# Kernel tuning notes

Measured on AMD Instinct MI355X. Metric: run time of the kernel, lower is better.

## Reference

```python
import jax, jax.numpy as jnp
from jax import lax
import numpy as np

H = 20  # hidden_size


def _lstm_layer(x, Wih, Whh, bih, bhh):
    # x: [B, T, D_in]; Wih: [4H, D_in]; Whh: [4H, H]
    B = x.shape[0]
    b = bih + bhh  # [4H]

    def step(carry, xt):
        h, c = carry
        gates = xt @ Wih.T + h @ Whh.T + b  # [B, 4H]
        i, f, g, o = jnp.split(gates, 4, axis=-1)  # torch gate order: i,f,g,o
        i = jax.nn.sigmoid(i)
        f = jax.nn.sigmoid(f)
        g = jnp.tanh(g)
        o = jax.nn.sigmoid(o)
        c = f * c + i * g
        h = o * jnp.tanh(c)
        return (h, c), h

    h0 = jnp.zeros((B, H), x.dtype)
    c0 = jnp.zeros((B, H), x.dtype)
    (_, _), hs = lax.scan(step, (h0, c0), jnp.swapaxes(x, 0, 1))  # hs: [T, B, H]
    return jnp.swapaxes(hs, 0, 1)  # [B, T, H]


def setup_inputs() -> dict:
    key = jax.random.key(0)
    ks = jax.random.split(key, 11)
    B, T, D = 4096, 512, 1
    s = 1.0 / np.sqrt(H)  # torch LSTM init scale
    u = lambda k, shp: jax.random.uniform(k, shp, jnp.float32, -s, s)
    return {
        "x": jax.random.normal(ks[0], (B, T, D), jnp.float32),
        "Wih0": u(ks[1], (4 * H, D)),
        "Whh0": u(ks[2], (4 * H, H)),
        "bih0": u(ks[3], (4 * H,)),
        "bhh0": u(ks[4], (4 * H,)),
        "Wih1": u(ks[5], (4 * H, H)),
        "Whh1": u(ks[6], (4 * H, H)),
        "bih1": u(ks[7], (4 * H,)),
        "bhh1": u(ks[8], (4 * H,)),
        "fcW": u(ks[9], (1, H)),
        "fcb": u(ks[10], (1,)),
    }


def reference(x, Wih0, Whh0, bih0, bhh0, Wih1, Whh1, bih1, bhh1, fcW, fcb):
    h1 = _lstm_layer(x, Wih0, Whh0, bih0, bhh0)   # [B, T, H]
    h2 = _lstm_layer(h1, Wih1, Whh1, bih1, bhh1)  # [B, T, H]
    # self.drop is defined but never applied in the original forward
    return h2[:, -1, :] @ fcW.T + fcb  # [B, 1]
```

## Files before the change

kernel.cpp:

```cpp
#include <hip/hip_runtime.h>
#include <hip/hip_bf16.h>


namespace {
constexpr int H_  = 20;
constexpr int T_  = 512;
constexpr int B_  = 4096;
constexpr int GPB = 3;

typedef float __attribute__((ext_vector_type(2))) f32x2;

__device__ __forceinline__ float rcp_fast(float v) {
    return __builtin_amdgcn_rcpf(v);
}
__device__ __forceinline__ float sigm(float v) {
    return rcp_fast(1.0f + __expf(-v));
}
__device__ __forceinline__ float tanh_fast(float v) {
    return fmaf(-2.0f, rcp_fast(1.0f + __expf(2.0f * v)), 1.0f);
}
__device__ __forceinline__ void pk_mac(f32x2& acc, f32x2 a, f32x2 b) {
#if __has_builtin(__builtin_amdgcn_pk_fma_f32)
    acc = __builtin_amdgcn_pk_fma_f32(a, b, acc);
#else
    asm("v_pk_fma_f32 %0, %1, %2, %0" : "+v"(acc) : "v"(a), "v"(b));
#endif
}
}

__global__ __launch_bounds__(256, 3) void lstm2_fc_kernel(
    const float* __restrict__ x,
    const float* __restrict__ Wih0, const float* __restrict__ Whh0,
    const float* __restrict__ bih0, const float* __restrict__ bhh0,
    const float* __restrict__ Wih1, const float* __restrict__ Whh1,
    const float* __restrict__ bih1, const float* __restrict__ bhh1,
    const float* __restrict__ fcW,  const float* __restrict__ fcb,
    float* __restrict__ out)
{
    const int tid  = threadIdx.x;
    const int w_s  = __builtin_amdgcn_readfirstlane(tid >> 6);
    const int lane = tid & 63;
    const int g    = lane / H_;
    const int j    = lane - g * H_;
    const int b    = blockIdx.x * GPB + g;
    const bool st  = (g < GPB) && (b < B_);
    const int  gx  = (g < GPB) ? g : (GPB - 1);

    __shared__ float xs[GPB][T_ + 2];
    __shared__ __align__(8)  f32x2 actP[2][4][64];
    __shared__ __align__(16) float h0s[4][4][28];
    __shared__ __align__(16) float h1s[4][4][28];

    {
        const int base_b = blockIdx.x * GPB;
        for (int idx = tid; idx < GPB * T_; idx += 256) {
            const int gg = idx >> 9;
            const int tt = idx & (T_ - 1);
            int row = base_b + gg; if (row >= B_) row = B_ - 1;
            xs[gg][tt] = x[(size_t)row * T_ + tt];
        }
        if (tid < GPB * 2) xs[tid >> 1][T_ + (tid & 1)] = 0.0f;
    }

    const int r = w_s * H_ + j;
    float w0x   = Wih0[r];
    float bias0 = bih0[r] + bhh0[r];
    float bias1 = bih1[r] + bhh1[r];
    f32x2 w0hP[10], w1iP[10], w1hP[10];
    #pragma unroll
    for (int m = 0; m < 10; ++m) {
        f32x2 a = { Whh0[r * H_ + 2*m], Whh0[r * H_ + 2*m + 1] };
        f32x2 c = { Wih1[r * H_ + 2*m], Wih1[r * H_ + 2*m + 1] };
        f32x2 d = { Whh1[r * H_ + 2*m], Whh1[r * H_ + 2*m + 1] };
        w0hP[m] = a; w1iP[m] = c; w1hP[m] = d;
    }
    asm volatile("" : "+v"(w0x), "+v"(bias0), "+v"(bias1));
    #pragma unroll
    for (int m = 0; m < 10; ++m) {
        asm volatile("" : "+v"(w0hP[m]), "+v"(w1iP[m]), "+v"(w1hP[m]));
    }

    f32x2 h0p[10], h1p[10];
    #pragma unroll
    for (int m = 0; m < 10; ++m) {
        f32x2 z = {0.0f, 0.0f};
        h0p[m] = z; h1p[m] = z;
    }
    float c0 = 0.0f, c1 = 0.0f;

    const float4* h0row = reinterpret_cast<const float4*>(&h0s[w_s][gx][0]);
    const float4* h1row = reinterpret_cast<const float4*>(&h1s[w_s][gx][0]);
    const float*  xrow  = &xs[gx][0];

    __syncthreads();
    float xv = xrow[0];

    #pragma unroll 1
    for (int t = 0; t <= T_; ++t) {
        const int par = t & 1;
        f32x2 sA = {0.f, 0.f}, sB = {0.f, 0.f};
        f32x2 uA = {0.f, 0.f}, uB = {0.f, 0.f};
        f32x2 vA = {0.f, 0.f}, vB = {0.f, 0.f};
        #pragma unroll
        for (int m = 0; m < 10; m += 2) {
            pk_mac(sA, w0hP[m    ], h0p[m    ]);
            pk_mac(sB, w0hP[m + 1], h0p[m + 1]);
            pk_mac(uA, w1iP[m    ], h0p[m    ]);
            pk_mac(uB, w1iP[m + 1], h0p[m + 1]);
            pk_mac(vA, w1hP[m    ], h1p[m    ]);
            pk_mac(vB, w1hP[m + 1], h1p[m + 1]);
        }
        const float gate0 = fmaf(w0x, xv, bias0) + ((sA.x + sA.y) + (sB.x + sB.y));
        const float gate1 = (bias1 + ((uA.x + uA.y) + (uB.x + uB.y)))
                          + ((vA.x + vA.y) + (vB.x + vB.y));
        float a0, a1;
        if (w_s == 2) { a0 = tanh_fast(gate0); a1 = tanh_fast(gate1); }
        else          { a0 = sigm(gate0);      a1 = sigm(gate1); }
        f32x2 aw = { a0, a1 };
        actP[par][w_s][lane] = aw;
        const float xnext = xrow[t + 1];
        __syncthreads();

        const f32x2 i01 = actP[par][0][lane];
        const f32x2 f01 = actP[par][1][lane];
        const f32x2 z01 = actP[par][2][lane];
        const f32x2 o01 = actP[par][3][lane];

        c0 = fmaf(f01.x, c0, i01.x * z01.x);
        const float h0n = o01.x * tanh_fast(c0);
        const float keep = (t == 0) ? 0.0f : 1.0f;
        c1 = fmaf(f01.y, c1, i01.y * z01.y) * keep;
        const float h1n = o01.y * tanh_fast(c1);

        h0s[w_s][g][j] = h0n;
        h1s[w_s][g][j] = h1n;
        #pragma unroll
        for (int c4 = 0; c4 < 5; ++c4) {
            const float4 v0 = h0row[c4];
            f32x2 p0a = { v0.x, v0.y }, p0b = { v0.z, v0.w };
            h0p[2*c4] = p0a; h0p[2*c4+1] = p0b;
            const float4 v1 = h1row[c4];
            f32x2 p1a = { v1.x, v1.y }, p1b = { v1.z, v1.w };
            h1p[2*c4] = p1a; h1p[2*c4+1] = p1b;
        }

        xv = xnext;
    }

    if (w_s == 0 && st && j == 0) {
        float acc = fcb[0];
        #pragma unroll
        for (int m = 0; m < 10; ++m) {
            acc = fmaf(fcW[2*m    ], h1p[m].x, acc);
            acc = fmaf(fcW[2*m + 1], h1p[m].y, acc);
        }
        out[b] = acc;
    }
}

extern "C" void kernel_launch(void* const* d_in, const int* in_sizes, int n_in,
                              void* d_out, int out_size, void* d_ws, size_t ws_size,
                              hipStream_t stream) {
    const float* x    = (const float*)d_in[0];
    const float* Wih0 = (const float*)d_in[1];
    const float* Whh0 = (const float*)d_in[2];
    const float* bih0 = (const float*)d_in[3];
    const float* bhh0 = (const float*)d_in[4];
    const float* Wih1 = (const float*)d_in[5];
    const float* Whh1 = (const float*)d_in[6];
    const float* bih1 = (const float*)d_in[7];
    const float* bhh1 = (const float*)d_in[8];
    const float* fcW  = (const float*)d_in[9];
    const float* fcb  = (const float*)d_in[10];
    float* out = (float*)d_out;

    const int grid = (B_ + GPB - 1) / GPB;
    lstm2_fc_kernel<<<dim3(grid), dim3(256), 0, stream>>>(
        x, Wih0, Whh0, bih0, bhh0, Wih1, Whh1, bih1, bhh1, fcW, fcb, out);
}
```

Measured before the change: 687.7 us.

## Split LSTM layers across separate wavefronts in a pipelined 512-thread block

Layer 0 and layer 1 now run on separate sets of four wavefronts in one 512-thread block instead of each wave computing both layers. Layer 1 trails layer 0 by two steps, reading the layer-0 hidden state through a double-buffered shared array. The aim is to cut the per-step work and register load on the critical path of each wave. The cost is twice as many waves per batch group, a serial chain of 514 block-wide barriers over 8 waves, and more LDS traffic for the hidden-state exchange.

```diff
diff --git a/kernel.cpp b/kernel.cpp
--- a/kernel.cpp
+++ b/kernel.cpp
@@ -3,10 +3,11 @@
 
 
 namespace {
-constexpr int H_  = 20;
-constexpr int T_  = 512;
-constexpr int B_  = 4096;
-constexpr int GPB = 3;
+constexpr int H_    = 20;
+constexpr int T_    = 512;
+constexpr int B_    = 4096;
+constexpr int GPB   = 3;
+constexpr int NITER = T_ + 2;
 
 typedef float __attribute__((ext_vector_type(2))) f32x2;
 
@@ -28,7 +29,7 @@
 }
 }
 
-__global__ __launch_bounds__(256, 3) void lstm2_fc_kernel(
+__global__ __launch_bounds__(512, 4) void lstm2_fc_kernel(
     const float* __restrict__ x,
     const float* __restrict__ Wih0, const float* __restrict__ Whh0,
     const float* __restrict__ bih0, const float* __restrict__ bhh0,
@@ -38,122 +39,153 @@
     float* __restrict__ out)
 {
     const int tid  = threadIdx.x;
-    const int w_s  = __builtin_amdgcn_readfirstlane(tid >> 6);
+    const int wv   = __builtin_amdgcn_readfirstlane(tid >> 6);
+    const int isL1 = wv >> 2;
+    const int w_s  = wv & 3;
     const int lane = tid & 63;
     const int g    = lane / H_;
     const int j    = lane - g * H_;
     const int b    = blockIdx.x * GPB + g;
-    const bool st  = (g < GPB) && (b < B_);
-    const int  gx  = (g < GPB) ? g : (GPB - 1);
-
-    __shared__ float xs[GPB][T_ + 2];
-    __shared__ __align__(8)  f32x2 actP[2][4][64];
-    __shared__ __align__(16) float h0s[4][4][28];
-    __shared__ __align__(16) float h1s[4][4][28];
+    const int gx   = (g < GPB) ? g : (GPB - 1);
+
+    __shared__ float xs[GPB][T_];
+    __shared__ float act0[2][4][64];
+    __shared__ float act1[2][4][64];
+    __shared__ __align__(16) float h0priv[4][4][28];
+    __shared__ __align__(16) float h0shar[2][4][28];
+    __shared__ __align__(16) float h1priv[4][4][28];
 
     {
         const int base_b = blockIdx.x * GPB;
-        for (int idx = tid; idx < GPB * T_; idx += 256) {
+        for (int idx = tid; idx < GPB * T_; idx += 512) {
             const int gg = idx >> 9;
             const int tt = idx & (T_ - 1);
             int row = base_b + gg; if (row >= B_) row = B_ - 1;
             xs[gg][tt] = x[(size_t)row * T_ + tt];
         }
-        if (tid < GPB * 2) xs[tid >> 1][T_ + (tid & 1)] = 0.0f;
+        float* hz = &h0priv[0][0][0];
+        (void)hz;
+        for (int idx = tid; idx < 4 * 4 * 28; idx += 512) (&h0priv[0][0][0])[idx] = 0.0f;
+        for (int idx = tid; idx < 2 * 4 * 28; idx += 512) (&h0shar[0][0][0])[idx] = 0.0f;
+        for (int idx = tid; idx < 4 * 4 * 28; idx += 512) (&h1priv[0][0][0])[idx] = 0.0f;
     }
 
     const int r = w_s * H_ + j;
-    float w0x   = Wih0[r];
-    float bias0 = bih0[r] + bhh0[r];
-    float bias1 = bih1[r] + bhh1[r];
-    f32x2 w0hP[10], w1iP[10], w1hP[10];
+    float w0x = 0.0f, bias = 0.0f;
+    f32x2 wA[10], wB[10];
+    if (!isL1) {
+        w0x  = Wih0[r];
+        bias = bih0[r] + bhh0[r];
+        #pragma unroll
+        for (int m = 0; m < 10; ++m) {
+            f32x2 a = { Whh0[r * H_ + 2*m], Whh0[r * H_ + 2*m + 1] };
+            wA[m] = a;
+            f32x2 z = { 0.0f, 0.0f }; wB[m] = z;
+        }
+    } else {
+        bias = bih1[r] + bhh1[r];
+        #pragma unroll
+        for (int m = 0; m < 10; ++m) {
+            f32x2 a = { Wih1[r * H_ + 2*m], Wih1[r * H_ + 2*m + 1] };
+            f32x2 c = { Whh1[r * H_ + 2*m], Whh1[r * H_ + 2*m + 1] };
+            wA[m] = a; wB[m] = c;
+        }
+    }
+    asm volatile("" : "+v"(w0x), "+v"(bias));
     #pragma unroll
-    for (int m = 0; m < 10; ++m) {
-        f32x2 a = { Whh0[r * H_ + 2*m], Whh0[r * H_ + 2*m + 1] };
-        f32x2 c = { Wih1[r * H_ + 2*m], Wih1[r * H_ + 2*m + 1] };
-        f32x2 d = { Whh1[r * H_ + 2*m], Whh1[r * H_ + 2*m + 1] };
-        w0hP[m] = a; w1iP[m] = c; w1hP[m] = d;
-    }
-    asm volatile("" : "+v"(w0x), "+v"(bias0), "+v"(bias1));
-    #pragma unroll
-    for (int m = 0; m < 10; ++m) {
-        asm volatile("" : "+v"(w0hP[m]), "+v"(w1iP[m]), "+v"(w1hP[m]));
-    }
-
-    f32x2 h0p[10], h1p[10];
-    #pragma unroll
-    for (int m = 0; m < 10; ++m) {
-        f32x2 z = {0.0f, 0.0f};
-        h0p[m] = z; h1p[m] = z;
-    }
-    float c0 = 0.0f, c1 = 0.0f;
-
-    const float4* h0row = reinterpret_cast<const float4*>(&h0s[w_s][gx][0]);
-    const float4* h1row = reinterpret_cast<const float4*>(&h1s[w_s][gx][0]);
-    const float*  xrow  = &xs[gx][0];
+    for (int m = 0; m < 10; ++m) asm volatile("" : "+v"(wA[m]), "+v"(wB[m]));
+
+    float cst = 0.0f;
+
+    const float4* h0privR = reinterpret_cast<const float4*>(&h0priv[w_s][gx][0]);
+    const float4* h1privR = reinterpret_cast<const float4*>(&h1priv[w_s][gx][0]);
 
     __syncthreads();
-    float xv = xrow[0];
 
     #pragma unroll 1
-    for (int t = 0; t <= T_; ++t) {
-        const int par = t & 1;
-        f32x2 sA = {0.f, 0.f}, sB = {0.f, 0.f};
-        f32x2 uA = {0.f, 0.f}, uB = {0.f, 0.f};
-        f32x2 vA = {0.f, 0.f}, vB = {0.f, 0.f};
-        #pragma unroll
-        for (int m = 0; m < 10; m += 2) {
-            pk_mac(sA, w0hP[m    ], h0p[m    ]);
-            pk_mac(sB, w0hP[m + 1], h0p[m + 1]);
-            pk_mac(uA, w1iP[m    ], h0p[m    ]);
-            pk_mac(uB, w1iP[m + 1], h0p[m + 1]);
-            pk_mac(vA, w1hP[m    ], h1p[m    ]);
-            pk_mac(vB, w1hP[m + 1], h1p[m + 1]);
-        }
-        const float gate0 = fmaf(w0x, xv, bias0) + ((sA.x + sA.y) + (sB.x + sB.y));
-        const float gate1 = (bias1 + ((uA.x + uA.y) + (uB.x + uB.y)))
-                          + ((vA.x + vA.y) + (vB.x + vB.y));
-        float a0, a1;
-        if (w_s == 2) { a0 = tanh_fast(gate0); a1 = tanh_fast(gate1); }
-        else          { a0 = sigm(gate0);      a1 = sigm(gate1); }
-        f32x2 aw = { a0, a1 };
-        actP[par][w_s][lane] = aw;
-        const float xnext = xrow[t + 1];
+    for (int i = 0; i < NITER; ++i) {
+        const int par = i & 1;
+
+        if (!isL1) {
+            if (i < T_) {
+                f32x2 hp[10];
+                #pragma unroll
+                for (int c4 = 0; c4 < 5; ++c4) {
+                    const float4 v = h0privR[c4];
+                    f32x2 pa = { v.x, v.y }, pb = { v.z, v.w };
+                    hp[2*c4] = pa; hp[2*c4+1] = pb;
+                }
+                f32x2 sA = {0.f,0.f}, sB = {0.f,0.f};
+                #pragma unroll
+                for (int m = 0; m < 10; m += 2) {
+                    pk_mac(sA, wA[m    ], hp[m    ]);
+                    pk_mac(sB, wA[m + 1], hp[m + 1]);
+                }
+                const float xv = xs[gx][i];
+                const float gate = fmaf(w0x, xv, bias)
+                                 + ((sA.x + sA.y) + (sB.x + sB.y));
+                const float a = (w_s == 2) ? tanh_fast(gate) : sigm(gate);
+                act0[par][w_s][lane] = a;
+            }
+        } else {
+            if (i >= 2) {
+                f32x2 h0p[10], h1p[10];
+                const float4* h0sh = reinterpret_cast<const float4*>(&h0shar[par][gx][0]);
+                #pragma unroll
+                for (int c4 = 0; c4 < 5; ++c4) {
+                    const float4 v0 = h0sh[c4];
+                    f32x2 a0 = { v0.x, v0.y }, b0 = { v0.z, v0.w };
+                    h0p[2*c4] = a0; h0p[2*c4+1] = b0;
+                    const float4 v1 = h1privR[c4];
+                    f32x2 a1 = { v1.x, v1.y }, b1 = { v1.z, v1.w };
+                    h1p[2*c4] = a1; h1p[2*c4+1] = b1;
+                }
+                f32x2 uA = {0.f,0.f}, uB = {0.f,0.f};
+                f32x2 vA = {0.f,0.f}, vB = {0.f,0.f};
+                #pragma unroll
+                for (int m = 0; m < 10; m += 2) {
+                    pk_mac(uA, wA[m    ], h0p[m    ]);
+                    pk_mac(uB, wA[m + 1], h0p[m + 1]);
+                    pk_mac(vA, wB[m    ], h1p[m    ]);
+                    pk_mac(vB, wB[m + 1], h1p[m + 1]);
+                }
+                const float gate = (bias + ((uA.x + uA.y) + (uB.x + uB.y)))
+                                 + ((vA.x + vA.y) + (vB.x + vB.y));
+                const float a = (w_s == 2) ? tanh_fast(gate) : sigm(gate);
+                act1[par][w_s][lane] = a;
+            }
+        }
+
         __syncthreads();
 
-        const f32x2 i01 = actP[par][0][lane];
-        const f32x2 f01 = actP[par][1][lane];
-        const f32x2 z01 = actP[par][2][lane];
-        const f32x2 o01 = actP[par][3][lane];
-
-        c0 = fmaf(f01.x, c0, i01.x * z01.x);
-        const float h0n = o01.x * tanh_fast(c0);
-        const float keep = (t == 0) ? 0.0f : 1.0f;
-        c1 = fmaf(f01.y, c1, i01.y * z01.y) * keep;
-        const float h1n = o01.y * tanh_fast(c1);
-
-        h0s[w_s][g][j] = h0n;
-        h1s[w_s][g][j] = h1n;
-        #pragma unroll
-        for (int c4 = 0; c4 < 5; ++c4) {
-            const float4 v0 = h0row[c4];
-            f32x2 p0a = { v0.x, v0.y }, p0b = { v0.z, v0.w };
-            h0p[2*c4] = p0a; h0p[2*c4+1] = p0b;
-            const float4 v1 = h1row[c4];
-            f32x2 p1a = { v1.x, v1.y }, p1b = { v1.z, v1.w };
-            h1p[2*c4] = p1a; h1p[2*c4+1] = p1b;
-        }
-
-        xv = xnext;
-    }
-
-    if (w_s == 0 && st && j == 0) {
+        if (!isL1) {
+            if (i < T_) {
+                const float iv = act0[par][0][lane];
+                const float fv = act0[par][1][lane];
+                const float zv = act0[par][2][lane];
+                const float ov = act0[par][3][lane];
+                cst = fmaf(fv, cst, iv * zv);
+                const float hn = ov * tanh_fast(cst);
+                h0priv[w_s][g][j] = hn;
+                if (w_s == 0) h0shar[par][g][j] = hn;
+            }
+        } else {
+            if (i >= 2) {
+                const float iv = act1[par][0][lane];
+                const float fv = act1[par][1][lane];
+                const float zv = act1[par][2][lane];
+                const float ov = act1[par][3][lane];
+                cst = fmaf(fv, cst, iv * zv);
+                const float hn = ov * tanh_fast(cst);
+                h1priv[w_s][g][j] = hn;
+            }
+        }
+    }
+
+    if (isL1 && w_s == 0 && g < GPB && j == 0 && b < B_) {
         float acc = fcb[0];
         #pragma unroll
-        for (int m = 0; m < 10; ++m) {
-            acc = fmaf(fcW[2*m    ], h1p[m].x, acc);
-            acc = fmaf(fcW[2*m + 1], h1p[m].y, acc);
-        }
+        for (int k = 0; k < H_; ++k) acc = fmaf(fcW[k], h1priv[0][g][k], acc);
         out[b] = acc;
     }
 }
@@ -175,6 +207,6 @@
     float* out = (float*)d_out;
 
     const int grid = (B_ + GPB - 1) / GPB;
-    lstm2_fc_kernel<<<dim3(grid), dim3(256), 0, stream>>>(
+    lstm2_fc_kernel<<<dim3(grid), dim3(512), 0, stream>>>(
         x, Wih0, Whh0, bih0, bhh0, Wih1, Whh1, bih1, bhh1, fcW, fcb, out);
 }
```

Result: slower. 950.4 us (+38.2%).
